# Optimization experiments

Measured on AMD Instinct MI355X. Metric: run time of the kernel, lower is better.

## Reference

```python
import jax, jax.numpy as jnp
import numpy as np

VOXEL_SIZE = 0.4
GAMMA = 1.1  # VoxelPointsSampler.GAMMA
PC_MIN, PC_MAX = -75.2, 75.2


def setup_inputs() -> dict:
    key = jax.random.key(0)
    ks = jax.random.split(key, 6)
    N, M, C, S = 200000, 256, 5, 128
    xy = jax.random.uniform(ks[0], (N, 2), minval=PC_MIN, maxval=PC_MAX)
    z = jax.random.uniform(ks[1], (N, 1), minval=-2.0, maxval=4.0)
    feat = jax.random.normal(ks[2], (N, C - 3))
    points = jnp.concatenate([xy, z, feat], axis=1)  # [N, 5]
    ctr = jax.random.uniform(ks[3], (M, 2), minval=PC_MIN * 0.9, maxval=PC_MAX * 0.9)
    cz = jnp.zeros((M, 1), jnp.float32)
    dims = jax.random.uniform(ks[4], (M, 3), minval=1.0, maxval=5.0)
    yaw = jax.random.uniform(ks[5], (M, 1), minval=-3.14, maxval=3.14)
    boxes = jnp.concatenate([ctr, cz, dims, yaw], axis=1)  # [M, 7]
    pc_start = jnp.array([PC_MIN, PC_MIN], dtype=jnp.float32)
    return {"points": points, "boxes": boxes, "pc_start": pc_start, "num_sample": S}


def reference(points, boxes, pc_start, num_sample):
    N, C = points.shape
    M = boxes.shape[0]
    # --- voxel-level radius ball query (distances in voxel units) ---
    pcoords = (points[:, :2] - pc_start) / VOXEL_SIZE          # [N, 2]
    qcoords = (boxes[:, :2] - pc_start) / VOXEL_SIZE           # [M, 2]
    r_vox = jnp.linalg.norm(boxes[:, 3:5] * 0.5, axis=-1) * GAMMA / VOXEL_SIZE  # [M]
    dist = jnp.linalg.norm(qcoords[:, None, :] - pcoords[None, :, :], axis=-1)  # [M, N]
    vmask = (dist < r_vox[:, None]).any(axis=0)                # [N]
    # --- cylindrical pool (metric space); invalid points pushed out of every radius ---
    BIG = jnp.asarray(1e6, points.dtype)
    xy_m = jnp.where(vmask[:, None], points[:, :2], BIG)       # [N, 2]
    radii = jnp.linalg.norm(boxes[:, 3:5] * 0.5, axis=-1) * GAMMA  # [M]
    dis = jnp.linalg.norm(boxes[:, None, :2] - xy_m[None, :, :], axis=-1)  # [M, N]
    pmask = (dis <= radii[:, None]).astype(points.dtype)       # 0/1 [M, N]
    sm, sidx = jax.lax.top_k(pmask, num_sample)                # [M, S]
    smb = sm > 0.5                                             # bool [M, S]
    # unique indices across all sampled slots (fixed-size for jit)
    uniq, inv = jnp.unique(sidx.ravel(), return_inverse=True,
                           size=M * num_sample, fill_value=0)
    query_points = points[uniq]                                # [M*S, C] (padded)
    sampled_points = points[sidx] * smb[:, :, None]            # [M, S, C]
    idx = inv.reshape(M, num_sample).astype(jnp.int32) * smb   # [M, S]
    return sampled_points, idx, query_points
```

## Files before the change

kernel.cpp:

```cpp
#include <hip/hip_runtime.h>

typedef unsigned long long u64;
typedef unsigned int u32;
typedef unsigned short u16;
typedef unsigned char u8;

#define VOX 0.4f
#define GAM 1.1f
#define NCX 16
#define CELLW 32.0f
#define CAP 64

__device__ __forceinline__ float dist2d(float ax, float ay, float bx, float by) {
  float dx = __fsub_rn(ax, bx);
  float dy = __fsub_rn(ay, by);
  return __fsqrt_rn(__fadd_rn(__fmul_rn(dx, dx), __fmul_rn(dy, dy)));
}

__device__ __forceinline__ float box_radius(const float* __restrict__ boxes, int m) {
  float hx = __fmul_rn(boxes[m * 7 + 3], 0.5f);
  float hy = __fmul_rn(boxes[m * 7 + 4], 0.5f);
  float nr = __fsqrt_rn(__fadd_rn(__fmul_rn(hx, hx), __fmul_rn(hy, hy)));
  return __fmul_rn(nr, GAM);
}

__device__ __forceinline__ void box_voxel(const float* __restrict__ boxes, int m,
                                          float psx, float psy,
                                          float& qx, float& qy, float& r) {
  qx = __fdiv_rn(__fsub_rn(boxes[m * 7 + 0], psx), VOX);
  qy = __fdiv_rn(__fsub_rn(boxes[m * 7 + 1], psy), VOX);
  float hx = __fmul_rn(boxes[m * 7 + 3], 0.5f);
  float hy = __fmul_rn(boxes[m * 7 + 4], 0.5f);
  float nr = __fsqrt_rn(__fadd_rn(__fmul_rn(hx, hx), __fmul_rn(hy, hy)));
  r = __fdiv_rn(__fmul_rn(nr, GAM), VOX);
}

__global__ void k_prep(const float* __restrict__ boxes, const float* __restrict__ pc_start,
                       float* __restrict__ qxv, float* __restrict__ qyv, float* __restrict__ rv,
                       int* __restrict__ cellCnt, u16* __restrict__ cellList, int M) {
  const int tid = threadIdx.x;
  if (blockIdx.x == 0) {
    for (int m = tid; m < M; m += 256) {
      float qx, qy, r;
      box_voxel(boxes, m, pc_start[0], pc_start[1], qx, qy, r);
      qxv[m] = qx; qyv[m] = qy; rv[m] = r;
    }
    return;
  }
  const int cell = blockIdx.x - 1;
  const int cx = cell & (NCX - 1), cy = cell >> 4;
  const int wv = tid >> 6, lane = tid & 63;
  __shared__ int wcnt[4];
  const float x0 = (cx == 0) ? -3e38f : cx * CELLW;
  const float x1 = (cx == NCX - 1) ? 3e38f : (cx + 1) * CELLW;
  const float y0 = (cy == 0) ? -3e38f : cy * CELLW;
  const float y1 = (cy == NCX - 1) ? 3e38f : (cy + 1) * CELLW;
  bool hit = false;
  if (tid < M) {
    float qx, qy, r;
    box_voxel(boxes, tid, pc_start[0], pc_start[1], qx, qy, r);
    float ddx = fmaxf(0.0f, fmaxf(x0 - qx, qx - x1));
    float ddy = fmaxf(0.0f, fmaxf(y0 - qy, qy - y1));
    float rr = r + 0.01f;
    hit = (ddx * ddx + ddy * ddy <= rr * rr);
  }
  u64 b = __ballot(hit);
  if (lane == 0) wcnt[wv] = __popcll(b);
  __syncthreads();
  int base = 0;
  for (int w = 0; w < wv; ++w) base += wcnt[w];
  if (hit) {
    int slot = base + __popcll(b & ((1ULL << lane) - 1ULL));
    if (slot < CAP) cellList[cell * CAP + slot] = (u16)tid;
  }
  if (tid == 0) cellCnt[cell] = wcnt[0] + wcnt[1] + wcnt[2] + wcnt[3];
}

__global__ void k_vmask_count(const float* __restrict__ pts, const float* __restrict__ boxes,
                              const float* __restrict__ qxv, const float* __restrict__ qyv,
                              const float* __restrict__ rv,
                              const int* __restrict__ cellCnt, const u16* __restrict__ cellList,
                              u64* __restrict__ vbits, u8* __restrict__ present,
                              u64* __restrict__ bmG, int* __restrict__ cpng,
                              const float* __restrict__ pc_start,
                              int N, int M) {
  __shared__ float cpx[256], cpy[256];
  __shared__ int cpn[256];
  __shared__ int ccell[256];
  __shared__ float sbx[256], sby[256], sbr[256];
  __shared__ u64 bm[256][4];
  __shared__ int wcnt[4];
  const int tid = threadIdx.x;
  const int blk = blockIdx.x;
  const int n = blk * 256 + tid;
  const int wv = tid >> 6, lane = tid & 63;
  const float psx = pc_start[0], psy = pc_start[1];
  const bool valid = (n < N);

  bm[tid][0] = 0; bm[tid][1] = 0; bm[tid][2] = 0; bm[tid][3] = 0;
  if (tid < M) {
    sbx[tid] = boxes[tid * 7 + 0];
    sby[tid] = boxes[tid * 7 + 1];
    sbr[tid] = box_radius(boxes, tid);
  }

  float px = 1e6f, py = 1e6f, pvx = 0.f, pvy = 0.f;
  if (valid) {
    px = pts[n * 5 + 0];
    py = pts[n * 5 + 1];
    pvx = __fdiv_rn(__fsub_rn(px, psx), VOX);
    pvy = __fdiv_rn(__fsub_rn(py, psy), VOX);
    present[n] = 0;
  }

  bool flag = false;
  int mycell = 0;
  if (valid) {
    int cx = (int)floorf(pvx * (1.0f / CELLW));
    int cy = (int)floorf(pvy * (1.0f / CELLW));
    cx = cx < 0 ? 0 : (cx > NCX - 1 ? NCX - 1 : cx);
    cy = cy < 0 ? 0 : (cy > NCX - 1 ? NCX - 1 : cy);
    mycell = cy * NCX + cx;
    const int k = cellCnt[mycell];
    if (k <= CAP) {
      for (int j = 0; j < k; ++j) {
        const int m = cellList[mycell * CAP + j];
        float d = dist2d(qxv[m], qyv[m], pvx, pvy);
        if (d < rv[m]) { flag = true; break; }
      }
    } else {
      for (int m = 0; m < M; ++m) {
        float d = dist2d(qxv[m], qyv[m], pvx, pvy);
        if (d < rv[m]) { flag = true; break; }
      }
    }
  }
  u64 b = __ballot(flag);
  if (lane == 0) {
    vbits[n >> 6] = b;
    wcnt[wv] = __popcll(b);
  }
  __syncthreads();

  int base = 0;
  for (int w = 0; w < wv; ++w) base += wcnt[w];
  if (flag) {
    int slot = base + __popcll(b & ((1ULL << lane) - 1ULL));
    cpx[slot] = px;
    cpy[slot] = py;
    cpn[slot] = n;
    ccell[slot] = mycell;
  }
  __syncthreads();
  const int nfl = wcnt[0] + wcnt[1] + wcnt[2] + wcnt[3];
  if (tid < nfl) cpng[blk * 256 + tid] = cpn[tid];

  if (tid < nfl) {
    const float mx = cpx[tid], my = cpy[tid];
    const int cell = ccell[tid];
    const int k = cellCnt[cell];
    const u64 bit = 1ULL << (tid & 63);
    const int word = tid >> 6;
    if (k <= CAP) {
      for (int j = 0; j < k; ++j) {
        const int m = cellList[cell * CAP + j];
        float d = dist2d(sbx[m], sby[m], mx, my);
        if (d <= sbr[m]) atomicOr(&bm[m][word], bit);
      }
    } else {
      for (int m = 0; m < M; ++m) {
        float d = dist2d(sbx[m], sby[m], mx, my);
        if (d <= sbr[m]) atomicOr(&bm[m][word], bit);
      }
    }
  }
  __syncthreads();

  if (tid < M) {
    u64* dst = bmG + ((size_t)blk * M + tid) * 4;
    dst[0] = bm[tid][0]; dst[1] = bm[tid][1];
    dst[2] = bm[tid][2]; dst[3] = bm[tid][3];
  }
}

__global__ void __launch_bounds__(1024) k_scanfill(
    const float* __restrict__ pts, const float* __restrict__ boxes,
    const u64* __restrict__ bmG, const int* __restrict__ cpng,
    const u64* __restrict__ vbits, int* __restrict__ kcount,
    int* __restrict__ sidx, u8* __restrict__ present,
    int N, int M, int S, int nchunk) {
  const int m = blockIdx.x;
  const int t = threadIdx.x;
  const int lane = t & 63, wv = t >> 6;
  __shared__ int wsum[16];
  __shared__ int zws[16];

  u64 w0 = 0, w1 = 0, w2 = 0, w3 = 0;
  int v = 0;
  if (t < nchunk) {
    const u64* bp = bmG + ((size_t)t * M + m) * 4;
    w0 = bp[0]; w1 = bp[1]; w2 = bp[2]; w3 = bp[3];
    v = __popcll(w0) + __popcll(w1) + __popcll(w2) + __popcll(w3);
  }
  int incl = v;
  for (int d = 1; d < 64; d <<= 1) {
    int x = __shfl_up(incl, d);
    if (lane >= d) incl += x;
  }
  if (lane == 63) wsum[wv] = incl;
  __syncthreads();
  if (t < 16) {
    int s = wsum[t];
    for (int d = 1; d < 16; d <<= 1) {
      int x = __shfl_up(s, d);
      if (t >= d) s += x;
    }
    wsum[t] = s;
  }
  __syncthreads();
  const int wbase = (wv > 0) ? wsum[wv - 1] : 0;
  const int off = wbase + incl - v;
  const int total = wsum[15];
  const int k0 = total < S ? total : S;
  if (t == 0) kcount[m] = k0;

  if (t < nchunk && v > 0 && off < S) {
    const int* pbase = cpng + t * 256;
    int cum = off;
    u64 ws4[4] = {w0, w1, w2, w3};
    for (int wi = 0; wi < 4 && cum < S; ++wi) {
      u64 w = ws4[wi];
      while (w && cum < S) {
        int j = (wi << 6) + __builtin_ctzll(w);
        w &= w - 1;
        int pn = pbase[j];
        sidx[m * S + cum] = pn;
        present[pn] = 1;
        ++cum;
      }
    }
  }

  if (k0 >= S) return;
  const float bx = boxes[m * 7 + 0], by = boxes[m * 7 + 1];
  const float r = box_radius(boxes, m);
  const u64 ltmask = (1ULL << lane) - 1ULL;
  int fill = k0;
  for (int p0 = 0; p0 < N && fill < S; p0 += 1024) {
    const int n = p0 + t;
    const bool validn = n < N;
    bool one = false;
    if (validn) {
      u64 wbit = vbits[n >> 6];
      if ((wbit >> (n & 63)) & 1ULL) {
        float d = dist2d(bx, by, pts[n * 5 + 0], pts[n * 5 + 1]);
        one = (d <= r);
      }
    }
    const bool z = validn && !one;
    u64 b = __ballot(z);
    if (lane == 0) zws[wv] = __popcll(b);
    __syncthreads();
    int zbase = 0, ztot = 0;
    for (int ww = 0; ww < 16; ++ww) {
      int c = zws[ww];
      if (ww < wv) zbase += c;
      ztot += c;
    }
    if (z) {
      int pos = fill + zbase + __popcll(b & ltmask);
      if (pos < S) { sidx[m * S + pos] = n; present[n] = 1; }
    }
    fill += ztot;
    __syncthreads();
  }
}

__global__ void k_pres2bits(const u8* __restrict__ present, u64* __restrict__ pbits,
                            int* __restrict__ csum, int N) {
  const int tid = threadIdx.x;
  const int blk = blockIdx.x;
  const int n = blk * 256 + tid;
  const int wv = tid >> 6, lane = tid & 63;
  __shared__ int ws[4];
  const bool f = (n < N) && present[n];
  u64 b = __ballot(f);
  if (lane == 0) {
    pbits[blk * 4 + wv] = b;
    ws[wv] = __popcll(b);
  }
  __syncthreads();
  if (tid == 0) csum[blk] = ws[0] + ws[1] + ws[2] + ws[3];
}

__global__ void __launch_bounds__(1024) k_scan(const int* __restrict__ csum,
                                               int* __restrict__ boff, int nb) {
  __shared__ int wsum[16];
  const int t = threadIdx.x, lane = t & 63, wv = t >> 6;
  int v = (t < nb) ? csum[t] : 0;
  int incl = v;
  for (int d = 1; d < 64; d <<= 1) {
    int x = __shfl_up(incl, d);
    if (lane >= d) incl += x;
  }
  if (lane == 63) wsum[wv] = incl;
  __syncthreads();
  if (t < 16) {
    int s = wsum[t];
    for (int d = 1; d < 16; d <<= 1) {
      int x = __shfl_up(s, d);
      if (t >= d) s += x;
    }
    wsum[t] = s;
  }
  __syncthreads();
  const int base = (wv > 0) ? wsum[wv - 1] : 0;
  if (t < nb) boff[t] = base + incl - v;
  if (t == 0) boff[1024] = wsum[15];
}

__global__ void k_outpad(const float* __restrict__ pts, const int* __restrict__ sidx,
                         const int* __restrict__ kcount, const u64* __restrict__ pbits,
                         const int* __restrict__ boff,
                         float* __restrict__ out_samp, float* __restrict__ out_idx,
                         float* __restrict__ out_query, int MS, int S) {
  const int e = blockIdx.x * 256 + threadIdx.x;
  if (e >= MS) return;
  const int U = boff[1024];
  if (e >= U) {
    float* q = out_query + (size_t)e * 5;
    q[0] = pts[0]; q[1] = pts[1]; q[2] = pts[2]; q[3] = pts[3]; q[4] = pts[4];
  }
  const int m = e / S;
  const int s = e - m * S;
  const int n = sidx[e];
  const int c = n >> 8, w = n >> 6;
  int rank = boff[c];
  for (int k = c * 4; k < w; ++k) rank += __popcll(pbits[k]);
  rank += __popcll(pbits[w] & ((1ULL << (n & 63)) - 1ULL));
  const float* p = pts + (size_t)n * 5;
  float* q = out_query + (size_t)rank * 5;
  q[0] = p[0]; q[1] = p[1]; q[2] = p[2]; q[3] = p[3]; q[4] = p[4];
  float* o = out_samp + (size_t)e * 5;
  if (s < kcount[m]) {
    o[0] = p[0]; o[1] = p[1]; o[2] = p[2]; o[3] = p[3]; o[4] = p[4];
    out_idx[e] = (float)rank;
  } else {
    o[0] = 0.f; o[1] = 0.f; o[2] = 0.f; o[3] = 0.f; o[4] = 0.f;
    out_idx[e] = 0.f;
  }
}

extern "C" void kernel_launch(void* const* d_in, const int* in_sizes, int n_in,
                              void* d_out, int out_size, void* d_ws, size_t ws_size,
                              hipStream_t stream) {
  const float* pts = (const float*)d_in[0];
  const float* boxes = (const float*)d_in[1];
  const float* pc_start = (const float*)d_in[2];
  const int N = in_sizes[0] / 5;
  const int M = in_sizes[1] / 7;
  const int S = out_size / (M * 11);
  const int MS = M * S;

  float* out_samp = (float*)d_out;
  float* out_idx = out_samp + (size_t)MS * 5;
  float* out_query = out_idx + (size_t)MS;

  const int nb = (N + 255) / 256;
  const int nchunk = nb;

  char* w = (char*)d_ws;
  auto take = [&](size_t bytes) {
    char* p = w;
    w += (bytes + 15) & ~(size_t)15;
    return (void*)p;
  };
  u64* vbits     = (u64*)take((size_t)(nb * 4) * 8);
  u64* pbits     = (u64*)take((size_t)(nb * 4) * 8);
  u64* bmG       = (u64*)take((size_t)nchunk * M * 4 * 8);
  int* cpng      = (int*)take((size_t)nchunk * 256 * 4);
  int* sidx      = (int*)take((size_t)MS * 4);
  int* kcount    = (int*)take((size_t)M * 4);
  int* csum      = (int*)take((size_t)1024 * 4);
  int* boff      = (int*)take((size_t)1025 * 4);
  u8*  present   = (u8*)take((size_t)N);
  float* qxv     = (float*)take((size_t)M * 4);
  float* qyv     = (float*)take((size_t)M * 4);
  float* rv      = (float*)take((size_t)M * 4);
  int* cellCnt   = (int*)take((size_t)NCX * NCX * 4);
  u16* cellList  = (u16*)take((size_t)NCX * NCX * CAP * 2);

  k_prep<<<NCX * NCX + 1, 256, 0, stream>>>(boxes, pc_start, qxv, qyv, rv,
                                            cellCnt, cellList, M);
  k_vmask_count<<<nb, 256, 0, stream>>>(pts, boxes, qxv, qyv, rv, cellCnt, cellList,
                                        vbits, present, bmG, cpng, pc_start, N, M);
  k_scanfill<<<M, 1024, 0, stream>>>(pts, boxes, bmG, cpng, vbits, kcount,
                                     sidx, present, N, M, S, nchunk);
  k_pres2bits<<<nb, 256, 0, stream>>>(present, pbits, csum, N);
  k_scan<<<1, 1024, 0, stream>>>(csum, boff, nb);
  k_outpad<<<(MS + 255) / 256, 256, 0, stream>>>(pts, sidx, kcount, pbits, boff,
                                                 out_samp, out_idx, out_query, MS, S);
}
```

Measured before the change: 90.12 us.

## Fuse presence bitmap, block scan and output gather into one kernel

Replaces the three tail kernels (presence-to-bits, single-block scan, output pad/gather) with one kernel. Every 1024-thread block rebuilds the full presence bitmap and chunk prefix sums in shared memory, then computes ranks and writes the outputs. This removes two kernel launches and the global round trips for pbits, csum and boff. In exchange each of the 32 blocks redundantly reads all N presence bytes, and the fixed NW64=3200 shared array caps N at about 204800 points.

```diff
diff --git a/kernel.cpp b/kernel.cpp
--- a/kernel.cpp
+++ b/kernel.cpp
@@ -276,28 +276,31 @@
   }
 }
 
-__global__ void k_pres2bits(const u8* __restrict__ present, u64* __restrict__ pbits,
-                            int* __restrict__ csum, int N) {
-  const int tid = threadIdx.x;
-  const int blk = blockIdx.x;
-  const int n = blk * 256 + tid;
-  const int wv = tid >> 6, lane = tid & 63;
-  __shared__ int ws[4];
-  const bool f = (n < N) && present[n];
-  u64 b = __ballot(f);
-  if (lane == 0) {
-    pbits[blk * 4 + wv] = b;
-    ws[wv] = __popcll(b);
-  }
-  __syncthreads();
-  if (tid == 0) csum[blk] = ws[0] + ws[1] + ws[2] + ws[3];
-}
-
-__global__ void __launch_bounds__(1024) k_scan(const int* __restrict__ csum,
-                                               int* __restrict__ boff, int nb) {
+#define NW64 3200
+__global__ void __launch_bounds__(1024) k_out(
+    const float* __restrict__ pts, const int* __restrict__ sidx,
+    const int* __restrict__ kcount, const u8* __restrict__ present,
+    float* __restrict__ out_samp, float* __restrict__ out_idx,
+    float* __restrict__ out_query, int N, int MS, int S, int nchunk) {
+  __shared__ u64 shp[NW64];
+  __shared__ int shb[1024];
   __shared__ int wsum[16];
   const int t = threadIdx.x, lane = t & 63, wv = t >> 6;
-  int v = (t < nb) ? csum[t] : 0;
+  const int nw = nchunk * 4;
+
+  for (int i = wv; i < nw; i += 16) {
+    const int n = i * 64 + lane;
+    const bool f = (n < N) && present[n];
+    u64 b = __ballot(f);
+    if (lane == 0) shp[i] = b;
+  }
+  __syncthreads();
+
+  int v = 0;
+  if (t < nchunk) {
+    const u64* p = &shp[t * 4];
+    v = __popcll(p[0]) + __popcll(p[1]) + __popcll(p[2]) + __popcll(p[3]);
+  }
   int incl = v;
   for (int d = 1; d < 64; d <<= 1) {
     int x = __shfl_up(incl, d);
@@ -314,19 +317,12 @@
     wsum[t] = s;
   }
   __syncthreads();
-  const int base = (wv > 0) ? wsum[wv - 1] : 0;
-  if (t < nb) boff[t] = base + incl - v;
-  if (t == 0) boff[1024] = wsum[15];
-}
-
-__global__ void k_outpad(const float* __restrict__ pts, const int* __restrict__ sidx,
-                         const int* __restrict__ kcount, const u64* __restrict__ pbits,
-                         const int* __restrict__ boff,
-                         float* __restrict__ out_samp, float* __restrict__ out_idx,
-                         float* __restrict__ out_query, int MS, int S) {
-  const int e = blockIdx.x * 256 + threadIdx.x;
+  shb[t] = ((wv > 0) ? wsum[wv - 1] : 0) + incl - v;
+  const int U = wsum[15];
+  __syncthreads();
+
+  const int e = blockIdx.x * 1024 + t;
   if (e >= MS) return;
-  const int U = boff[1024];
   if (e >= U) {
     float* q = out_query + (size_t)e * 5;
     q[0] = pts[0]; q[1] = pts[1]; q[2] = pts[2]; q[3] = pts[3]; q[4] = pts[4];
@@ -335,9 +331,9 @@
   const int s = e - m * S;
   const int n = sidx[e];
   const int c = n >> 8, w = n >> 6;
-  int rank = boff[c];
-  for (int k = c * 4; k < w; ++k) rank += __popcll(pbits[k]);
-  rank += __popcll(pbits[w] & ((1ULL << (n & 63)) - 1ULL));
+  int rank = shb[c];
+  for (int k = c * 4; k < w; ++k) rank += __popcll(shp[k]);
+  rank += __popcll(shp[w] & ((1ULL << (n & 63)) - 1ULL));
   const float* p = pts + (size_t)n * 5;
   float* q = out_query + (size_t)rank * 5;
   q[0] = p[0]; q[1] = p[1]; q[2] = p[2]; q[3] = p[3]; q[4] = p[4];
@@ -376,13 +372,10 @@
     return (void*)p;
   };
   u64* vbits     = (u64*)take((size_t)(nb * 4) * 8);
-  u64* pbits     = (u64*)take((size_t)(nb * 4) * 8);
   u64* bmG       = (u64*)take((size_t)nchunk * M * 4 * 8);
   int* cpng      = (int*)take((size_t)nchunk * 256 * 4);
   int* sidx      = (int*)take((size_t)MS * 4);
   int* kcount    = (int*)take((size_t)M * 4);
-  int* csum      = (int*)take((size_t)1024 * 4);
-  int* boff      = (int*)take((size_t)1025 * 4);
   u8*  present   = (u8*)take((size_t)N);
   float* qxv     = (float*)take((size_t)M * 4);
   float* qyv     = (float*)take((size_t)M * 4);
@@ -396,8 +389,7 @@
                                         vbits, present, bmG, cpng, pc_start, N, M);
   k_scanfill<<<M, 1024, 0, stream>>>(pts, boxes, bmG, cpng, vbits, kcount,
                                      sidx, present, N, M, S, nchunk);
-  k_pres2bits<<<nb, 256, 0, stream>>>(present, pbits, csum, N);
-  k_scan<<<1, 1024, 0, stream>>>(csum, boff, nb);
-  k_outpad<<<(MS + 255) / 256, 256, 0, stream>>>(pts, sidx, kcount, pbits, boff,
-                                                 out_samp, out_idx, out_query, MS, S);
-}
+  k_out<<<(MS + 1023) / 1024, 1024, 0, stream>>>(pts, sidx, kcount, present,
+                                                 out_samp, out_idx, out_query,
+                                                 N, MS, S, nchunk);
+}
```

Result: slower. 154.5 us (+71.5%).
